# Kernel tuning notes

Hardware: AMD Instinct MI355X
Metric: run time of the kernel (lower is better)

The kernel has to match this reference:

```python
import jax, jax.numpy as jnp
import numpy as np

NUM_HEADS = 12


def setup_inputs() -> dict:
    key = jax.random.key(0)
    k1, k2, k3 = jax.random.split(key, 3)
    B, S, D = 8, 1024, 768
    x = jax.random.normal(k1, (B, S, D), dtype=jnp.float32)
    # Linear weights, torch convention [out_features, in_features], small init
    w_qkv = jax.random.normal(k2, (3 * D, D), dtype=jnp.float32) * 0.02
    b_qkv = jnp.zeros((3 * D,), dtype=jnp.float32)
    w_proj = jax.random.normal(k3, (D, D), dtype=jnp.float32) * 0.02
    b_proj = jnp.zeros((D,), dtype=jnp.float32)
    return {"x": x, "w_qkv": w_qkv, "b_qkv": b_qkv, "w_proj": w_proj, "b_proj": b_proj}


def reference(x, w_qkv, b_qkv, w_proj, b_proj):
    B, S, D = x.shape
    H = NUM_HEADS
    hd = D // H
    qkv = x @ w_qkv.T + b_qkv                      # [B, S, 3D]
    qkv = qkv.reshape(B, S, 3, H, hd).transpose(2, 0, 3, 1, 4)  # [3, B, H, S, hd]
    q, k, v = qkv[0], qkv[1], qkv[2]
    # NOTE: source computes self.scale but never applies it -> unscaled QK^T
    weights = jnp.einsum('bhqd,bhkd->bhqk', q, k)  # [B, H, S, S]
    attn = jax.nn.softmax(weights, axis=-1)        # dropout = 0 (eval)
    out = jnp.einsum('bhqk,bhkd->bhqd', attn, v)   # [B, H, S, hd]
    out = out.transpose(0, 2, 1, 3).reshape(B, S, D)
    return out @ w_proj.T + b_proj
```

## Files before the change

### kernel.cpp

```cpp
#include <hip/hip_runtime.h>


typedef short bf16x8 __attribute__((ext_vector_type(8)));
typedef float f32x4  __attribute__((ext_vector_type(4)));

#define MFMA16(a, b, c) __builtin_amdgcn_mfma_f32_16x16x32_bf16((a), (b), (c), 0, 0, 0)

__device__ __forceinline__ unsigned short f2bf(float f) {
    union { float f; unsigned int u; } v; v.f = f;
    unsigned int u = v.u;
    return (unsigned short)((u + 0x7fffu + ((u >> 16) & 1u)) >> 16);
}

__device__ __forceinline__ unsigned int cvt2(float x, float y) {
#if __has_builtin(__builtin_amdgcn_cvt_pk_bf16_f32)
    auto v = __builtin_amdgcn_cvt_pk_bf16_f32(x, y);
    unsigned int b; __builtin_memcpy(&b, &v, 4); return b;
#else
    return (unsigned int)f2bf(x) | ((unsigned int)f2bf(y) << 16);
#endif
}

__device__ __forceinline__ void gl2lds16(const unsigned short* g, unsigned short* l) {
    __builtin_amdgcn_global_load_lds(
        (const unsigned int __attribute__((address_space(1)))*)g,
        (unsigned int __attribute__((address_space(3)))*)l,
        16, 0, 0);
}

__global__ void cvt3_kernel(const float* __restrict__ x,
                            const float* __restrict__ wq,
                            const float* __restrict__ wp,
                            unsigned short* __restrict__ xb,
                            unsigned short* __restrict__ wqb,
                            unsigned short* __restrict__ wpb) {
    int i = blockIdx.x * 256 + threadIdx.x;
    const float* s; unsigned short* d; int off;
    if (i < 1572864)      { s = x;  d = xb;  off = i; }
    else if (i < 2015232) { s = wq; d = wqb; off = i - 1572864; }
    else                  { s = wp; d = wpb; off = i - 2015232; }
    float4 v = ((const float4*)s)[off];
    ushort4 o;
    o.x = f2bf(v.x); o.y = f2bf(v.y); o.z = f2bf(v.z); o.w = f2bf(v.w);
    ((ushort4*)d)[off] = o;
}

__global__ __launch_bounds__(512, 4) void gemm_qkv(
    const unsigned short* __restrict__ A,
    const unsigned short* __restrict__ Bm,
    const float* __restrict__ bias,
    unsigned short* __restrict__ Qo,
    unsigned short* __restrict__ Ko,
    unsigned short* __restrict__ Vto) {
    const int K = 768;
    __shared__ __align__(16) unsigned short smem[16384];
    unsigned short* const As0 = smem;
    unsigned short* const As1 = smem + 4096;
    unsigned short* const Bs0 = smem + 8192;
    unsigned short* const Bs1 = smem + 12288;
    const int tid = threadIdx.x;
    const int wave = tid >> 6, lane = tid & 63;
    const int quad = lane >> 4, l16 = lane & 15;
    const int wm = (wave >> 1) * 32, wn = (wave & 1) * 64;
    const int tileM = blockIdx.x * 128, tileN = blockIdx.y * 128;

    f32x4 zero4 = {0.f, 0.f, 0.f, 0.f};
    f32x4 acc[2][4];
#pragma unroll
    for (int i = 0; i < 2; ++i)
#pragma unroll
        for (int j = 0; j < 4; ++j) acc[i][j] = zero4;

    const int sr = tid >> 2, sc = tid & 3;
    const unsigned short* Ag = A + (size_t)(tileM + sr) * K + sc * 8;
    const unsigned short* Bg = Bm + (size_t)(tileN + sr) * K + sc * 8;
    const int sdst = wave << 9;

    auto compute = [&](const unsigned short* Ar, const unsigned short* Br) {
        bf16x8 af[2], bfr[4];
#pragma unroll
        for (int t = 0; t < 2; ++t)
            af[t] = *(const bf16x8*)(Ar + (wm + t * 16 + l16) * 32 + quad * 8);
#pragma unroll
        for (int t = 0; t < 4; ++t)
            bfr[t] = *(const bf16x8*)(Br + (wn + t * 16 + l16) * 32 + quad * 8);
#pragma unroll
        for (int tm = 0; tm < 2; ++tm)
#pragma unroll
            for (int tn = 0; tn < 4; ++tn)
                acc[tm][tn] = MFMA16(af[tm], bfr[tn], acc[tm][tn]);
    };

    gl2lds16(Ag, As0 + sdst);
    gl2lds16(Bg, Bs0 + sdst);
    for (int it = 0; it < 24; it += 2) {
        __syncthreads();
        {
            int k1 = (it + 1) << 5;
            gl2lds16(Ag + k1, As1 + sdst);
            gl2lds16(Bg + k1, Bs1 + sdst);
        }
        compute(As0, Bs0);
        __syncthreads();
        if (it + 2 < 24) {
            int k2 = (it + 2) << 5;
            gl2lds16(Ag + k2, As0 + sdst);
            gl2lds16(Bg + k2, Bs0 + sdst);
        }
        compute(As1, Bs1);
    }

    const int t = blockIdx.y / 6;
    if (t < 2) {
        const float scale = (t == 0) ? 1.44269504f : 1.0f;
        unsigned short* dst = (t == 0) ? Qo : Ko;
        const int nb = tileN - t * 768 + wn;
#pragma unroll
        for (int tm = 0; tm < 2; ++tm) {
#pragma unroll
            for (int tn = 0; tn < 4; ++tn) {
                int nl = nb + tn * 16 + l16;
                float bv = bias[tileN + wn + tn * 16 + l16];
#pragma unroll
                for (int r = 0; r < 4; ++r) {
                    int m = tileM + wm + tm * 16 + quad * 4 + r;
                    dst[(size_t)m * 768 + nl] = f2bf((acc[tm][tn][r] + bv) * scale);
                }
            }
        }
    } else {
        const int b = tileM >> 10, srow = tileM & 1023;
#pragma unroll
        for (int h2 = 0; h2 < 2; ++h2) {
            __syncthreads();
            if ((wave & 1) == h2) {
#pragma unroll
                for (int tn = 0; tn < 4; ++tn) {
                    int dl = tn * 16 + l16;
                    float bv = bias[tileN + h2 * 64 + dl];
#pragma unroll
                    for (int tm = 0; tm < 2; ++tm) {
                        int mb = wm + tm * 16 + quad * 4;
                        uint2 pk;
                        pk.x = cvt2(acc[tm][tn][0] + bv, acc[tm][tn][1] + bv);
                        pk.y = cvt2(acc[tm][tn][2] + bv, acc[tm][tn][3] + bv);
                        *(uint2*)(smem + dl * 136 + mb) = pk;
                    }
                }
            }
            __syncthreads();
#pragma unroll
            for (int pass = 0; pass < 2; ++pass) {
                int dl = pass * 32 + (tid >> 4), soff = (tid & 15) * 8;
                bf16x8 row = *(const bf16x8*)(smem + dl * 136 + soff);
                int rem = tileN + h2 * 64 + dl - 1536;
                int h = rem >> 6, d = rem & 63;
                *(bf16x8*)(Vto + (((size_t)b * 12 + h) * 64 + d) * 1024 + srow + soff) = row;
            }
        }
    }
}

__global__ __launch_bounds__(256) void attn_kernel(
    const unsigned short* __restrict__ Q,
    const unsigned short* __restrict__ Kg,
    const unsigned short* __restrict__ Vt,
    unsigned short* __restrict__ O) {
    __shared__ __align__(16) unsigned short smem[24576];
    unsigned short* Ps = smem;

    const int tid = threadIdx.x;
    const int wave = tid >> 6, lane = tid & 63;
    const int quad = lane >> 4, l16 = lane & 15;
    const int s4 = l16 & 3;
    const int qt = blockIdx.x;
    const int bh = blockIdx.y;
    const int b = bh / 12, h = bh - b * 12;

    const unsigned short* Qb = Q  + ((size_t)b * 1024 + qt * 128) * 768 + h * 64;
    const unsigned short* Kb = Kg + (size_t)b * 1024 * 768 + h * 64;
    const unsigned short* Vb = Vt + (size_t)bh * 64 * 1024;

    auto stageKV = [&](int kv0, int buf) {
        int r = tid >> 2, c = tid & 3;
        const unsigned short* gk = Kb + (size_t)(kv0 + r) * 768 + c * 8;
        const unsigned short* gv = Vb + (size_t)r * 1024 + kv0 + c * 8;
        unsigned short* Kd = smem + 8192 + buf * 4096;
        unsigned short* Vd = smem + 16384 + buf * 4096;
        int dst = (wave << 6) * 8;
        gl2lds16(gk,      Kd + dst);
        gl2lds16(gk + 32, Kd + 2048 + dst);
        gl2lds16(gv,      Vd + dst);
        gl2lds16(gv + 32, Vd + 2048 + dst);
    };

#pragma unroll
    for (int i = 0; i < 2; ++i) {
        int s = tid + (i << 8);
        int r = s >> 2, c = s & 3;
        const unsigned short* gq = Qb + (size_t)r * 768 + c * 8;
        int dst = ((wave << 6) + (i << 8)) * 8;
        gl2lds16(gq,      smem + dst);
        gl2lds16(gq + 32, smem + 4096 + dst);
    }
    stageKV(0, 0);
    __syncthreads();
    bf16x8 qf[2][2];
#pragma unroll
    for (int ks = 0; ks < 2; ++ks)
#pragma unroll
        for (int tq = 0; tq < 2; ++tq)
            qf[ks][tq] = *(const bf16x8*)(smem + ks * 4096 +
                                          (wave * 32 + tq * 16 + l16) * 32 + quad * 8);
    __syncthreads();

    f32x4 zero4 = {0.f, 0.f, 0.f, 0.f};
    f32x4 oacc[2][4];
    float rsum[2] = {0.f, 0.f};
#pragma unroll
    for (int tm = 0; tm < 2; ++tm)
#pragma unroll
        for (int tv = 0; tv < 4; ++tv) oacc[tm][tv] = zero4;

    for (int it = 0; it < 16; ++it) {
        if (it + 1 < 16) stageKV((it + 1) << 6, (it + 1) & 1);
        const unsigned short* Kr = smem + 8192 + (it & 1) * 4096;
        const unsigned short* Vr = smem + 16384 + (it & 1) * 4096;

        f32x4 st[4][2];
#pragma unroll
        for (int tk = 0; tk < 4; ++tk)
#pragma unroll
            for (int tq = 0; tq < 2; ++tq) st[tk][tq] = zero4;
#pragma unroll
        for (int ks = 0; ks < 2; ++ks) {
            bf16x8 kf[4];
#pragma unroll
            for (int tk = 0; tk < 4; ++tk)
                kf[tk] = *(const bf16x8*)(Kr + ks * 2048 + (tk * 16 + l16) * 32 + quad * 8);
#pragma unroll
            for (int tk = 0; tk < 4; ++tk)
#pragma unroll
                for (int tq = 0; tq < 2; ++tq)
                    st[tk][tq] = MFMA16(kf[tk], qf[ks][tq], st[tk][tq]);
        }

#pragma unroll
        for (int tq = 0; tq < 2; ++tq) {
            unsigned short* prp = Ps + (wave * 32 + tq * 16 + l16) * 64 + quad * 4;
#pragma unroll
            for (int tk = 0; tk < 4; ++tk) {
                float e0 = __builtin_amdgcn_exp2f(st[tk][tq][0]);
                float e1 = __builtin_amdgcn_exp2f(st[tk][tq][1]);
                float e2 = __builtin_amdgcn_exp2f(st[tk][tq][2]);
                float e3 = __builtin_amdgcn_exp2f(st[tk][tq][3]);
                rsum[tq] += (e0 + e1) + (e2 + e3);
                uint2 pk;
                pk.x = cvt2(e0, e1);
                pk.y = cvt2(e2, e3);
                *(uint2*)(prp + ((tk ^ s4) << 4)) = pk;
            }
        }

#pragma unroll
        for (int ks2 = 0; ks2 < 2; ++ks2) {
            bf16x8 ap[2], bv[4];
            int colswz = ((ks2 << 5) + (quad << 3)) ^ (s4 << 4);
#pragma unroll
            for (int tm = 0; tm < 2; ++tm)
                ap[tm] = *(const bf16x8*)(Ps + (wave * 32 + tm * 16 + l16) * 64 + colswz);
#pragma unroll
            for (int tv = 0; tv < 4; ++tv)
                bv[tv] = *(const bf16x8*)(Vr + ks2 * 2048 + (tv * 16 + l16) * 32 + quad * 8);
#pragma unroll
            for (int tm = 0; tm < 2; ++tm)
#pragma unroll
                for (int tv = 0; tv < 4; ++tv)
                    oacc[tm][tv] = MFMA16(ap[tm], bv[tv], oacc[tm][tv]);
        }
        __syncthreads();
    }

#pragma unroll
    for (int tq = 0; tq < 2; ++tq) {
        rsum[tq] += __shfl_xor(rsum[tq], 16, 64);
        rsum[tq] += __shfl_xor(rsum[tq], 32, 64);
    }
    float* sums = (float*)smem;
    if (quad == 0) {
        sums[wave * 32 + l16]      = rsum[0];
        sums[wave * 32 + 16 + l16] = rsum[1];
    }
    __syncthreads();

#pragma unroll
    for (int tm = 0; tm < 2; ++tm) {
        f32x4 inv;
#pragma unroll
        for (int r = 0; r < 4; ++r)
            inv[r] = 1.0f / sums[wave * 32 + tm * 16 + quad * 4 + r];
#pragma unroll
        for (int tv = 0; tv < 4; ++tv)
#pragma unroll
            for (int r = 0; r < 4; ++r) {
                int srow = qt * 128 + wave * 32 + tm * 16 + quad * 4 + r;
                int col = h * 64 + tv * 16 + l16;
                O[((size_t)b * 1024 + srow) * 768 + col] = f2bf(oacc[tm][tv][r] * inv[r]);
            }
    }
}

__global__ __launch_bounds__(512, 4) void gemm_proj(
    const unsigned short* __restrict__ A,
    const unsigned short* __restrict__ Bm,
    const float* __restrict__ bias,
    float* __restrict__ out) {
    const int K = 768;
    __shared__ __align__(16) unsigned short smem[16384];
    unsigned short* const As0 = smem;
    unsigned short* const As1 = smem + 4096;
    unsigned short* const Bs0 = smem + 8192;
    unsigned short* const Bs1 = smem + 12288;
    const int tid = threadIdx.x;
    const int wave = tid >> 6, lane = tid & 63;
    const int quad = lane >> 4, l16 = lane & 15;
    const int wm = (wave >> 1) * 32, wn = (wave & 1) * 64;
    const int tileM = blockIdx.x * 128, tileN = blockIdx.y * 128;

    f32x4 zero4 = {0.f, 0.f, 0.f, 0.f};
    f32x4 acc[2][4];
#pragma unroll
    for (int i = 0; i < 2; ++i)
#pragma unroll
        for (int j = 0; j < 4; ++j) acc[i][j] = zero4;

    const int sr = tid >> 2, sc = tid & 3;
    const unsigned short* Ag = A + (size_t)(tileM + sr) * K + sc * 8;
    const unsigned short* Bg = Bm + (size_t)(tileN + sr) * K + sc * 8;
    const int sdst = wave << 9;

    auto compute = [&](const unsigned short* Ar, const unsigned short* Br) {
        bf16x8 af[2], bfr[4];
#pragma unroll
        for (int t = 0; t < 2; ++t)
            af[t] = *(const bf16x8*)(Ar + (wm + t * 16 + l16) * 32 + quad * 8);
#pragma unroll
        for (int t = 0; t < 4; ++t)
            bfr[t] = *(const bf16x8*)(Br + (wn + t * 16 + l16) * 32 + quad * 8);
#pragma unroll
        for (int tm = 0; tm < 2; ++tm)
#pragma unroll
            for (int tn = 0; tn < 4; ++tn)
                acc[tm][tn] = MFMA16(af[tm], bfr[tn], acc[tm][tn]);
    };

    gl2lds16(Ag, As0 + sdst);
    gl2lds16(Bg, Bs0 + sdst);
    for (int it = 0; it < 24; it += 2) {
        __syncthreads();
        {
            int k1 = (it + 1) << 5;
            gl2lds16(Ag + k1, As1 + sdst);
            gl2lds16(Bg + k1, Bs1 + sdst);
        }
        compute(As0, Bs0);
        __syncthreads();
        if (it + 2 < 24) {
            int k2 = (it + 2) << 5;
            gl2lds16(Ag + k2, As0 + sdst);
            gl2lds16(Bg + k2, Bs0 + sdst);
        }
        compute(As1, Bs1);
    }

#pragma unroll
    for (int tm = 0; tm < 2; ++tm) {
#pragma unroll
        for (int tn = 0; tn < 4; ++tn) {
            int n = tileN + wn + tn * 16 + l16;
            float bv = bias[n];
#pragma unroll
            for (int r = 0; r < 4; ++r) {
                int m = tileM + wm + tm * 16 + quad * 4 + r;
                out[(size_t)m * 768 + n] = acc[tm][tn][r] + bv;
            }
        }
    }
}

extern "C" void kernel_launch(void* const* d_in, const int* in_sizes, int n_in,
                              void* d_out, int out_size, void* d_ws, size_t ws_size,
                              hipStream_t stream) {
    (void)in_sizes; (void)n_in; (void)out_size; (void)ws_size;
    const float* x      = (const float*)d_in[0];
    const float* w_qkv  = (const float*)d_in[1];
    const float* b_qkv  = (const float*)d_in[2];
    const float* w_proj = (const float*)d_in[3];
    const float* b_proj = (const float*)d_in[4];
    float* out = (float*)d_out;

    char* ws = (char*)d_ws;
    unsigned short* xb     = (unsigned short*)(ws + 0);
    unsigned short* wqkvb  = (unsigned short*)(ws + 12582912);
    unsigned short* wprojb = (unsigned short*)(ws + 16121856);
    unsigned short* Qw     = (unsigned short*)(ws + 17301504);
    unsigned short* Kw     = (unsigned short*)(ws + 29884416);
    unsigned short* Vtw    = (unsigned short*)(ws + 42467328);

    cvt3_kernel<<<8448, 256, 0, stream>>>(x, w_qkv, w_proj, xb, wqkvb, wprojb);
    gemm_qkv<<<dim3(64, 18), 512, 0, stream>>>(xb, wqkvb, b_qkv, Qw, Kw, Vtw);
    attn_kernel<<<dim3(8, 96), 256, 0, stream>>>(Qw, Kw, Vtw, xb);
    gemm_proj<<<dim3(64, 6), 512, 0, stream>>>(xb, wprojb, b_proj, out);
}
```

Measured before the change: 189.6 us.

## Keep softmax probabilities in registers and compute O transposed via 16x16x16 MFMA

The P·V product is restructured so the exponentiated scores stay in registers as bf16x4 B-operands. A 16x16x16 bf16 MFMA then computes O^T = V^T·P^T, which removes the P round-trip through shared memory and shrinks LDS from 48KB to 32KB. The row-sum reduction no longer goes through shared memory, and each lane writes packed 8-byte output stores. The trade-off is twice as many smaller-K MFMA instructions, plus an extra barrier at the top of each iteration.

```diff
diff --git a/kernel.cpp b/kernel.cpp
--- a/kernel.cpp
+++ b/kernel.cpp
@@ -2,9 +2,22 @@
 
 
 typedef short bf16x8 __attribute__((ext_vector_type(8)));
+typedef short bf16x4 __attribute__((ext_vector_type(4)));
 typedef float f32x4  __attribute__((ext_vector_type(4)));
 
 #define MFMA16(a, b, c) __builtin_amdgcn_mfma_f32_16x16x32_bf16((a), (b), (c), 0, 0, 0)
+
+#if __has_builtin(__builtin_amdgcn_mfma_f32_16x16x16bf16_1k)
+#define MFMAK16(a, b, c) __builtin_amdgcn_mfma_f32_16x16x16bf16_1k((a), (b), (c), 0, 0, 0)
+#elif __has_builtin(__builtin_amdgcn_mfma_f32_16x16x16_bf16)
+#define MFMAK16(a, b, c) __builtin_amdgcn_mfma_f32_16x16x16_bf16((a), (b), (c), 0, 0, 0)
+#else
+static __device__ __forceinline__ f32x4 mfmak16_asm(bf16x4 a, bf16x4 b, f32x4 c) {
+    asm volatile("v_mfma_f32_16x16x16_bf16 %0, %1, %2, %0" : "+v"(c) : "v"(a), "v"(b));
+    return c;
+}
+#define MFMAK16(a, b, c) mfmak16_asm((a), (b), (c))
+#endif
 
 __device__ __forceinline__ unsigned short f2bf(float f) {
     union { float f; unsigned int u; } v; v.f = f;
@@ -166,13 +179,11 @@
     const unsigned short* __restrict__ Kg,
     const unsigned short* __restrict__ Vt,
     unsigned short* __restrict__ O) {
-    __shared__ __align__(16) unsigned short smem[24576];
-    unsigned short* Ps = smem;
+    __shared__ __align__(16) unsigned short smem[16384];
 
     const int tid = threadIdx.x;
     const int wave = tid >> 6, lane = tid & 63;
     const int quad = lane >> 4, l16 = lane & 15;
-    const int s4 = l16 & 3;
     const int qt = blockIdx.x;
     const int bh = blockIdx.y;
     const int b = bh / 12, h = bh - b * 12;
@@ -185,8 +196,8 @@
         int r = tid >> 2, c = tid & 3;
         const unsigned short* gk = Kb + (size_t)(kv0 + r) * 768 + c * 8;
         const unsigned short* gv = Vb + (size_t)r * 1024 + kv0 + c * 8;
-        unsigned short* Kd = smem + 8192 + buf * 4096;
-        unsigned short* Vd = smem + 16384 + buf * 4096;
+        unsigned short* Kd = smem + buf * 4096;
+        unsigned short* Vd = smem + 8192 + buf * 4096;
         int dst = (wave << 6) * 8;
         gl2lds16(gk,      Kd + dst);
         gl2lds16(gk + 32, Kd + 2048 + dst);
@@ -203,7 +214,6 @@
         gl2lds16(gq,      smem + dst);
         gl2lds16(gq + 32, smem + 4096 + dst);
     }
-    stageKV(0, 0);
     __syncthreads();
     bf16x8 qf[2][2];
 #pragma unroll
@@ -213,19 +223,21 @@
             qf[ks][tq] = *(const bf16x8*)(smem + ks * 4096 +
                                           (wave * 32 + tq * 16 + l16) * 32 + quad * 8);
     __syncthreads();
+    stageKV(0, 0);
 
     f32x4 zero4 = {0.f, 0.f, 0.f, 0.f};
-    f32x4 oacc[2][4];
+    f32x4 ot[2][4];
     float rsum[2] = {0.f, 0.f};
 #pragma unroll
-    for (int tm = 0; tm < 2; ++tm)
-#pragma unroll
-        for (int tv = 0; tv < 4; ++tv) oacc[tm][tv] = zero4;
+    for (int tq = 0; tq < 2; ++tq)
+#pragma unroll
+        for (int dt = 0; dt < 4; ++dt) ot[tq][dt] = zero4;
 
     for (int it = 0; it < 16; ++it) {
+        __syncthreads();
         if (it + 1 < 16) stageKV((it + 1) << 6, (it + 1) & 1);
-        const unsigned short* Kr = smem + 8192 + (it & 1) * 4096;
-        const unsigned short* Vr = smem + 16384 + (it & 1) * 4096;
+        const unsigned short* Kr = smem + (it & 1) * 4096;
+        const unsigned short* Vr = smem + 8192 + (it & 1) * 4096;
 
         f32x4 st[4][2];
 #pragma unroll
@@ -245,40 +257,35 @@
                     st[tk][tq] = MFMA16(kf[tk], qf[ks][tq], st[tk][tq]);
         }
 
-#pragma unroll
-        for (int tq = 0; tq < 2; ++tq) {
-            unsigned short* prp = Ps + (wave * 32 + tq * 16 + l16) * 64 + quad * 4;
-#pragma unroll
-            for (int tk = 0; tk < 4; ++tk) {
+        bf16x4 pb[4][2];
+#pragma unroll
+        for (int tk = 0; tk < 4; ++tk)
+#pragma unroll
+            for (int tq = 0; tq < 2; ++tq) {
                 float e0 = __builtin_amdgcn_exp2f(st[tk][tq][0]);
                 float e1 = __builtin_amdgcn_exp2f(st[tk][tq][1]);
                 float e2 = __builtin_amdgcn_exp2f(st[tk][tq][2]);
                 float e3 = __builtin_amdgcn_exp2f(st[tk][tq][3]);
                 rsum[tq] += (e0 + e1) + (e2 + e3);
-                uint2 pk;
-                pk.x = cvt2(e0, e1);
-                pk.y = cvt2(e2, e3);
-                *(uint2*)(prp + ((tk ^ s4) << 4)) = pk;
+                union { unsigned int u[2]; bf16x4 v; } uu;
+                uu.u[0] = cvt2(e0, e1);
+                uu.u[1] = cvt2(e2, e3);
+                pb[tk][tq] = uu.v;
             }
-        }
-
-#pragma unroll
-        for (int ks2 = 0; ks2 < 2; ++ks2) {
-            bf16x8 ap[2], bv[4];
-            int colswz = ((ks2 << 5) + (quad << 3)) ^ (s4 << 4);
-#pragma unroll
-            for (int tm = 0; tm < 2; ++tm)
-                ap[tm] = *(const bf16x8*)(Ps + (wave * 32 + tm * 16 + l16) * 64 + colswz);
-#pragma unroll
-            for (int tv = 0; tv < 4; ++tv)
-                bv[tv] = *(const bf16x8*)(Vr + ks2 * 2048 + (tv * 16 + l16) * 32 + quad * 8);
-#pragma unroll
-            for (int tm = 0; tm < 2; ++tm)
-#pragma unroll
-                for (int tv = 0; tv < 4; ++tv)
-                    oacc[tm][tv] = MFMA16(ap[tm], bv[tv], oacc[tm][tv]);
-        }
-        __syncthreads();
+
+#pragma unroll
+        for (int tk = 0; tk < 4; ++tk) {
+            bf16x4 va[4];
+#pragma unroll
+            for (int dt = 0; dt < 4; ++dt)
+                va[dt] = *(const bf16x4*)(Vr + (tk >> 1) * 2048 +
+                                          (dt * 16 + l16) * 32 + (tk & 1) * 16 + quad * 4);
+#pragma unroll
+            for (int tq = 0; tq < 2; ++tq)
+#pragma unroll
+                for (int dt = 0; dt < 4; ++dt)
+                    ot[tq][dt] = MFMAK16(va[dt], pb[tk][tq], ot[tq][dt]);
+        }
     }
 
 #pragma unroll
@@ -286,27 +293,19 @@
         rsum[tq] += __shfl_xor(rsum[tq], 16, 64);
         rsum[tq] += __shfl_xor(rsum[tq], 32, 64);
     }
-    float* sums = (float*)smem;
-    if (quad == 0) {
-        sums[wave * 32 + l16]      = rsum[0];
-        sums[wave * 32 + 16 + l16] = rsum[1];
-    }
-    __syncthreads();
-
-#pragma unroll
-    for (int tm = 0; tm < 2; ++tm) {
-        f32x4 inv;
-#pragma unroll
-        for (int r = 0; r < 4; ++r)
-            inv[r] = 1.0f / sums[wave * 32 + tm * 16 + quad * 4 + r];
-#pragma unroll
-        for (int tv = 0; tv < 4; ++tv)
-#pragma unroll
-            for (int r = 0; r < 4; ++r) {
-                int srow = qt * 128 + wave * 32 + tm * 16 + quad * 4 + r;
-                int col = h * 64 + tv * 16 + l16;
-                O[((size_t)b * 1024 + srow) * 768 + col] = f2bf(oacc[tm][tv][r] * inv[r]);
-            }
+    float inv[2] = { 1.0f / rsum[0], 1.0f / rsum[1] };
+
+#pragma unroll
+    for (int tq = 0; tq < 2; ++tq) {
+        int srow = qt * 128 + wave * 32 + tq * 16 + l16;
+        unsigned short* orow = O + ((size_t)b * 1024 + srow) * 768 + h * 64 + quad * 4;
+#pragma unroll
+        for (int dt = 0; dt < 4; ++dt) {
+            uint2 pk;
+            pk.x = cvt2(ot[tq][dt][0] * inv[tq], ot[tq][dt][1] * inv[tq]);
+            pk.y = cvt2(ot[tq][dt][2] * inv[tq], ot[tq][dt][3] * inv[tq]);
+            *(uint2*)(orow + dt * 16) = pk;
+        }
     }
 }
 
```

Result: slower. 206.4 us (+8.9%).
